# Optimization experiments

Measured on AMD Instinct MI355X. Metric: run time of the kernel, lower is better.

Reference implementation:

```python
import jax, jax.numpy as jnp
import numpy as np

DIM = 768
ALL_KEY_DIM = 768
NUM_HEADS = 12
HEAD_DIM = DIM // NUM_HEADS
SCALE = HEAD_DIM ** -0.5


def setup_inputs() -> dict:
    key = jax.random.key(0)
    ks = jax.random.split(key, 8)
    B, N = 8, 1024
    s = 0.02
    return {
        "x": jax.random.normal(ks[0], (B, N, DIM), dtype=jnp.float32),
        "Wq": jax.random.normal(ks[1], (ALL_KEY_DIM, DIM), dtype=jnp.float32) * s,
        "Wk": jax.random.normal(ks[2], (ALL_KEY_DIM, DIM), dtype=jnp.float32) * s,
        "Wv": jax.random.normal(ks[3], (DIM, DIM), dtype=jnp.float32) * s,
        "bv": jnp.zeros((DIM,), dtype=jnp.float32),
        "Wmix": jax.random.normal(ks[4], (NUM_HEADS, ALL_KEY_DIM), dtype=jnp.float32) * s,
        "Wcb": jax.random.normal(ks[5], (NUM_HEADS, DIM), dtype=jnp.float32) * s,
        "Wproj": jax.random.normal(ks[6], (DIM, DIM), dtype=jnp.float32) * s,
        "bproj": jnp.zeros((DIM,), dtype=jnp.float32),
    }


def reference(x, Wq, Wk, Wv, bv, Wmix, Wcb, Wproj, bproj):
    B, N, C = x.shape
    H, Dh = NUM_HEADS, C // NUM_HEADS
    q_shared = x @ Wq.T                      # [B,N,Dk]
    k = x @ Wk.T                             # [B,N,Dk]
    v = (x @ Wv.T + bv).reshape(B, N, H, Dh).transpose(0, 2, 1, 3)  # [B,H,N,Dh]
    # per-head mixed query: q[b,h,n,d] = q_shared[b,n,d] * Wmix[h,d]
    q = jnp.einsum('bnd,hd->bhnd', q_shared, Wmix)
    # shared-key scores + content bias broadcast over query positions
    scores = jnp.einsum('bhnd,bmd->bhnm', q, k)          # [B,H,N,N]
    content_bias = jnp.einsum('bmd,hd->bhm', x, Wcb)     # [B,H,N]
    attn = jax.nn.softmax((scores + content_bias[:, :, None, :]) * SCALE, axis=-1)
    out = jnp.einsum('bhnm,bhmd->bhnd', attn, v)         # [B,H,N,Dh]
    out = out.transpose(0, 2, 1, 3).reshape(B, N, C)
    return out @ Wproj.T + bproj
```

## Files before the change

kernel.cpp:

```cpp
#include <hip/hip_runtime.h>
#include <stdint.h>

typedef unsigned short u16;
typedef unsigned char u8;
typedef unsigned long long u64;
typedef __attribute__((ext_vector_type(8))) short bf16x8;
typedef __attribute__((ext_vector_type(4))) float f32x4;

#define KLOG2E 0.18033688011112043f
#define QSCL 184.66496523378732f
#define SINV 0.0001220703125f
#define EXP2F(x) __builtin_amdgcn_exp2f(x)
#define WAITV(n) asm volatile("s_waitcnt vmcnt(" #n ")" ::: "memory")

__device__ __forceinline__ u16 f2bf(float f) {
  union { float f; unsigned u; } v; v.f = f;
  unsigned r = v.u + 0x7fffu + ((v.u >> 16) & 1u);
  return (u16)(r >> 16);
}
__device__ __forceinline__ float bf2f(u16 u) {
  union { unsigned u; float f; } v; v.u = ((unsigned)u) << 16;
  return v.f;
}
__device__ __forceinline__ u8 f2fp8(float f) {
  return (u8)(__builtin_amdgcn_cvt_pk_fp8_f32(f, f, 0, false) & 0xFF);
}
__device__ __forceinline__ long pk64(uint2 v) {
  return (long)(((u64)v.y << 32) | (u64)v.x);
}

__device__ __forceinline__ void gload16(const void* g, void* l) {
  __builtin_amdgcn_global_load_lds(
      (const __attribute__((address_space(1))) unsigned int*)g,
      (__attribute__((address_space(3))) unsigned int*)l, 16, 0, 0);
}

__global__ void cvt_f32_bf16(const float4* __restrict__ s, uint2* __restrict__ d, int n4) {
  int i = blockIdx.x * blockDim.x + threadIdx.x;
  int stride = gridDim.x * blockDim.x;
  for (; i < n4; i += stride) {
    float4 v = s[i];
    uint2 o;
    o.x = (unsigned)f2bf(v.x) | ((unsigned)f2bf(v.y) << 16);
    o.y = (unsigned)f2bf(v.z) | ((unsigned)f2bf(v.w) << 16);
    d[i] = o;
  }
}

template <int MODE>
__global__ __launch_bounds__(256, 2) void gemm_bt(
    const u16* __restrict__ A, const u16* __restrict__ Bm,
    void* __restrict__ Cp, void* __restrict__ Cp2,
    const float* __restrict__ bias, int ldc) {
  __shared__ u16 Ab[128 * 32];
  __shared__ u16 Bb[128 * 32];
  const int tid = threadIdx.x;
  const int l = tid & 63, w = tid >> 6;
  const int g = l >> 4, l15 = l & 15;
  const int wr = w >> 1, wc = w & 1;
  const int rowbase = blockIdx.y * 128, colbase = blockIdx.x * 128;

  f32x4 acc[4][4] = {};
  const char* Abase = (const char*)A + (size_t)rowbase * 1536;
  const char* Bbase = (const char*)Bm + (size_t)colbase * 1536;

  for (int kk = 0; kk < 768; kk += 32) {
    __syncthreads();
#pragma unroll
    for (int p = 0; p < 2; ++p) {
      int o = p * 4096 + w * 1024 + l * 16;
      int row = o >> 6, cb = o & 63;
      gload16(Abase + (size_t)row * 1536 + kk * 2 + cb, &Ab[(p * 4096 + w * 1024) / 2]);
      gload16(Bbase + (size_t)row * 1536 + kk * 2 + cb, &Bb[(p * 4096 + w * 1024) / 2]);
    }
    __syncthreads();
    bf16x8 af[4], bfr[4];
#pragma unroll
    for (int i = 0; i < 4; ++i) {
      af[i] = *(const bf16x8*)&Ab[(wr * 64 + i * 16 + l15) * 32 + g * 8];
      bfr[i] = *(const bf16x8*)&Bb[(wc * 64 + i * 16 + l15) * 32 + g * 8];
    }
#pragma unroll
    for (int mi = 0; mi < 4; ++mi)
#pragma unroll
      for (int ni = 0; ni < 4; ++ni)
        acc[mi][ni] = __builtin_amdgcn_mfma_f32_16x16x32_bf16(af[mi], bfr[ni], acc[mi][ni], 0, 0, 0);
  }

#pragma unroll
  for (int mi = 0; mi < 4; ++mi)
#pragma unroll
    for (int ni = 0; ni < 4; ++ni)
#pragma unroll
      for (int r = 0; r < 4; ++r) {
        int row = rowbase + wr * 64 + mi * 16 + g * 4 + r;
        int col = colbase + wc * 64 + ni * 16 + l15;
        float v = acc[mi][ni][r];
        if (MODE == 0) {
          if (col < 768) {
            ((u16*)Cp)[(size_t)row * 768 + col] = f2bf(v);
          } else {
            int d = col - 768;
            int chunk = d >> 7, w4 = (d >> 5) & 3, gg = (d >> 3) & 3, rr = d & 7;
            int dp = chunk * 128 + gg * 32 + w4 * 8 + rr;
            ((u8*)Cp2)[(size_t)row * 768 + dp] = f2fp8(v * 8.0f);
          }
        } else if (MODE == 2) {
          ((float*)Cp)[(size_t)row * ldc + col] = v + bias[col];
        } else {
          int b = col >> 10, nn = col & 1023;
          if (row < 768) {
            ((u16*)Cp)[(size_t)b * 786432 + (size_t)row * 1024 + nn] = f2bf(v + bias[row]);
          } else if (row < 780) {
            ((float*)Cp2)[(size_t)b * 12288 + (size_t)(row - 768) * 1024 + nn] = v * KLOG2E;
          }
        }
      }
}

__global__ __launch_bounds__(512, 6) void attn8(
    const u16* __restrict__ Qb,
    const u8* __restrict__ Kf8,
    const u16* __restrict__ vT,
    const float* __restrict__ cb,
    const float* __restrict__ Wmix,
    u16* __restrict__ OH)
{
  __shared__ u8 Kb[3][8192];
  __shared__ u16 Vb[2][4096];
  __shared__ u16 Pb[8][1024];

  const int gid = blockIdx.x;
  const int b = gid & 7;
  const int within = gid >> 3;
  const int h = within % 12, qt = within / 12;
  const int tid = threadIdx.x;
  const int l = tid & 63, w = tid >> 6;
  const int g = l >> 4, l15 = l & 15;

  const u8* Ksrc = Kf8 + (size_t)b * 786432;
  const char* Vsrc = (const char*)vT + (size_t)(b * 12 + h) * 131072;
  const float* cbp = cb + (size_t)(b * 12 + h) * 1024;

  uint2 qreg[24];
  {
    const u16* qrow = Qb + ((size_t)b * 1024 + qt * 128 + w * 16 + l15) * 768;
    const float* wmh = Wmix + h * 768;
#pragma unroll
    for (int wd = 0; wd < 24; ++wd) {
      bf16x8 qv = *(const bf16x8*)(qrow + wd * 32 + g * 8);
      const float* wm = wmh + wd * 32 + g * 8;
      float4 w0 = *(const float4*)wm;
      float4 w1 = *(const float4*)(wm + 4);
      float q0 = bf2f((u16)qv[0]) * (w0.x * QSCL);
      float q1 = bf2f((u16)qv[1]) * (w0.y * QSCL);
      float q2 = bf2f((u16)qv[2]) * (w0.z * QSCL);
      float q3 = bf2f((u16)qv[3]) * (w0.w * QSCL);
      float q4 = bf2f((u16)qv[4]) * (w1.x * QSCL);
      float q5 = bf2f((u16)qv[5]) * (w1.y * QSCL);
      float q6 = bf2f((u16)qv[6]) * (w1.z * QSCL);
      float q7 = bf2f((u16)qv[7]) * (w1.w * QSCL);
      int a = __builtin_amdgcn_cvt_pk_fp8_f32(q0, q1, 0, false);
      a = __builtin_amdgcn_cvt_pk_fp8_f32(q2, q3, a, true);
      int b2 = __builtin_amdgcn_cvt_pk_fp8_f32(q4, q5, 0, false);
      b2 = __builtin_amdgcn_cvt_pk_fp8_f32(q6, q7, b2, true);
      qreg[wd].x = (unsigned)a;
      qreg[wd].y = (unsigned)b2;
    }
  }

  auto STK = [&](int kt, int ch, int buf) {
    int o = tid * 16;
    int row = o >> 7, t = (o >> 4) & 7;
    gload16(Ksrc + (size_t)(kt * 64 + row) * 768 + ch * 128 + ((t ^ (row & 7)) * 16),
            (char*)Kb[buf] + o);
  };
  auto STV = [&](int kt, int buf) {
    int o = tid * 16;
    int kwin = o >> 12, o2 = o & 4095, d = o2 >> 6, s = (o2 >> 4) & 3;
    gload16(Vsrc + (size_t)d * 2048 + (kt * 64 + kwin * 32 + ((s ^ (d & 3)) * 8)) * 2,
            (char*)Vb[buf] + o);
  };

  float m_run = -1e30f, lpart = 0.f;
  f32x4 oacc[4] = {};
  STK(0, 0, 0);
  STK(0, 1, 1);
  STV(0, 0);
  __syncthreads();

  for (int kt = 0; kt < 16; ++kt) {
    f32x4 sa[4] = {};
#pragma unroll
    for (int ch = 0; ch < 6; ++ch) {
      if (ch == 1 && kt < 15) STV(kt + 1, (kt + 1) & 1);
      if (ch <= 3) STK(kt, ch + 2, (ch + 2) % 3);
      else if (kt < 15) STK(kt + 1, ch - 4, (ch + 2) % 3);
      __builtin_amdgcn_s_setprio(1);
#pragma unroll
      for (int j = 0; j < 2; ++j) {
        long qf0 = pk64(qreg[ch * 4 + 2 * j]);
        long qf1 = pk64(qreg[ch * 4 + 2 * j + 1]);
        int slot = (2 * g + j) ^ (l15 & 7);
#pragma unroll
        for (int s = 0; s < 4; ++s) {
          uint4 kk = *(const uint4*)&Kb[ch % 3][(16 * s + l15) * 128 + slot * 16];
          long klo = (long)(((u64)kk.y << 32) | kk.x);
          long khi = (long)(((u64)kk.w << 32) | kk.z);
          sa[s] = __builtin_amdgcn_mfma_f32_16x16x32_fp8_fp8(klo, qf0, sa[s], 0, 0, 0);
          sa[s] = __builtin_amdgcn_mfma_f32_16x16x32_fp8_fp8(khi, qf1, sa[s], 0, 0, 0);
        }
      }
      __builtin_amdgcn_s_setprio(0);
      if (ch == 1) {
        if (kt < 15) WAITV(2); else WAITV(1);
      } else if (ch >= 4) {
        if (kt < 15) WAITV(1); else WAITV(0);
      } else {
        WAITV(1);
      }
      __builtin_amdgcn_s_barrier();
    }

    float fv[16];
    float pmax = -1e30f;
#pragma unroll
    for (int s = 0; s < 4; ++s) {
      float4 cbv = *(const float4*)(cbp + kt * 64 + s * 16 + g * 4);
      fv[s * 4 + 0] = fmaf(sa[s][0], SINV, cbv.x);
      fv[s * 4 + 1] = fmaf(sa[s][1], SINV, cbv.y);
      fv[s * 4 + 2] = fmaf(sa[s][2], SINV, cbv.z);
      fv[s * 4 + 3] = fmaf(sa[s][3], SINV, cbv.w);
#pragma unroll
      for (int r = 0; r < 4; ++r) pmax = fmaxf(pmax, fv[s * 4 + r]);
    }
    pmax = fmaxf(pmax, __shfl_xor(pmax, 16));
    pmax = fmaxf(pmax, __shfl_xor(pmax, 32));
    if (__ballot(pmax > m_run)) {
      float mnew = fmaxf(m_run, pmax);
      float alpha = EXP2F(m_run - mnew);
      lpart *= alpha;
#pragma unroll
      for (int vf = 0; vf < 4; ++vf) oacc[vf] *= alpha;
      m_run = mnew;
    }
    float rs = 0.f;
#pragma unroll
    for (int r = 0; r < 16; ++r) {
      fv[r] = EXP2F(fv[r] - m_run);
      rs += fv[r];
    }
    rs += __shfl_xor(rs, 16);
    rs += __shfl_xor(rs, 32);
    lpart += rs;

#pragma unroll
    for (int s = 0; s < 4; ++s) {
      unsigned w01, w23;
      asm("v_cvt_pk_bf16_f32 %0, %1, %2" : "=v"(w01) : "v"(fv[s * 4]), "v"(fv[s * 4 + 1]));
      asm("v_cvt_pk_bf16_f32 %0, %1, %2" : "=v"(w23) : "v"(fv[s * 4 + 2]), "v"(fv[s * 4 + 3]));
      int ts = (2 * s + (g >> 1)) ^ (l15 & 7);
      uint2 uu; uu.x = w01; uu.y = w23;
      *(uint2*)((char*)Pb[w] + l15 * 128 + ts * 16 + (g & 1) * 8) = uu;
    }

#pragma unroll
    for (int kwin = 0; kwin < 2; ++kwin) {
      int tr = (4 * kwin + g) ^ (l15 & 7);
      bf16x8 pf = *(const bf16x8*)((const char*)Pb[w] + l15 * 128 + tr * 16);
#pragma unroll
      for (int vf = 0; vf < 4; ++vf) {
        int d = vf * 16 + l15;
        bf16x8 vfrag = *(const bf16x8*)((const char*)Vb[kt & 1] + kwin * 4096 + d * 64 +
                                        ((g ^ (d & 3)) * 16));
        oacc[vf] = __builtin_amdgcn_mfma_f32_16x16x32_bf16(vfrag, pf, oacc[vf], 0, 0, 0);
      }
    }
  }

  float rdiv = 1.f / lpart;
  size_t nrow = ((size_t)b * 1024 + qt * 128 + w * 16 + l15) * 768;
#pragma unroll
  for (int vf = 0; vf < 4; ++vf) {
    u64 pk = (u64)f2bf(oacc[vf][0] * rdiv) |
             ((u64)f2bf(oacc[vf][1] * rdiv) << 16) |
             ((u64)f2bf(oacc[vf][2] * rdiv) << 32) |
             ((u64)f2bf(oacc[vf][3] * rdiv) << 48);
    *(u64*)&OH[nrow + h * 64 + vf * 16 + 4 * g] = pk;
  }
}

static inline int cvtblocks(int n4) {
  int nb = (n4 + 255) / 256;
  return nb > 2048 ? 2048 : nb;
}

extern "C" void kernel_launch(void* const* d_in, const int* in_sizes, int n_in,
                              void* d_out, int out_size, void* d_ws, size_t ws_size,
                              hipStream_t stream) {
  (void)in_sizes; (void)n_in; (void)out_size; (void)ws_size;
  const float* x = (const float*)d_in[0];
  const float* Wq = (const float*)d_in[1];
  const float* Wk = (const float*)d_in[2];
  const float* Wv = (const float*)d_in[3];
  const float* bv = (const float*)d_in[4];
  const float* Wmix = (const float*)d_in[5];
  const float* Wcb = (const float*)d_in[6];
  const float* Wproj = (const float*)d_in[7];
  const float* bproj = (const float*)d_in[8];
  float* out = (float*)d_out;

  char* ws = (char*)d_ws;
  u16* xbf = (u16*)(ws);
  u16* Wqk = (u16*)(ws + 12582912);
  u16* Wvcb = (u16*)(ws + 14942208);
  u16* Wpj = (u16*)(ws + 16318464);
  u16* Qb = (u16*)(ws + 17498112);
  u8* Kf8 = (u8*)(ws + 30081024);
  u16* vT = (u16*)(ws + 36372480);
  float* cbb = (float*)(ws + 48955392);
  u16* OH = (u16*)(ws + 49348608);

  cvt_f32_bf16<<<cvtblocks(1572864), 256, 0, stream>>>((const float4*)x, (uint2*)xbf, 1572864);
  cvt_f32_bf16<<<cvtblocks(147456), 256, 0, stream>>>((const float4*)Wq, (uint2*)Wqk, 147456);
  cvt_f32_bf16<<<cvtblocks(147456), 256, 0, stream>>>((const float4*)Wk, (uint2*)(Wqk + 589824), 147456);
  cvt_f32_bf16<<<cvtblocks(147456), 256, 0, stream>>>((const float4*)Wv, (uint2*)Wvcb, 147456);
  cvt_f32_bf16<<<cvtblocks(2304), 256, 0, stream>>>((const float4*)Wcb, (uint2*)(Wvcb + 589824), 2304);
  cvt_f32_bf16<<<cvtblocks(147456), 256, 0, stream>>>((const float4*)Wproj, (uint2*)Wpj, 147456);

  gemm_bt<0><<<dim3(12, 64), 256, 0, stream>>>(xbf, Wqk, Qb, Kf8, nullptr, 0);
  gemm_bt<1><<<dim3(64, 7), 256, 0, stream>>>(Wvcb, xbf, vT, cbb, bv, 0);
  attn8<<<dim3(768), 512, 0, stream>>>(Qb, Kf8, vT, cbb, Wmix, OH);
  gemm_bt<2><<<dim3(6, 64), 256, 0, stream>>>(OH, Wpj, out, nullptr, bproj, 768);
}
```

Measured before the change: 246.2 us.

## Rewrite attention with 32x32 scaled fp8 and bf16 MFMAs in registers

```diff
diff --git a/kernel.cpp b/kernel.cpp
--- a/kernel.cpp
+++ b/kernel.cpp
@@ -6,6 +6,8 @@
 typedef unsigned long long u64;
 typedef __attribute__((ext_vector_type(8))) short bf16x8;
 typedef __attribute__((ext_vector_type(4))) float f32x4;
+typedef __attribute__((ext_vector_type(16))) float f32x16;
+typedef __attribute__((ext_vector_type(8))) int i32x8;
 
 #define KLOG2E 0.18033688011112043f
 #define QSCL 184.66496523378732f
@@ -24,9 +26,6 @@
 }
 __device__ __forceinline__ u8 f2fp8(float f) {
   return (u8)(__builtin_amdgcn_cvt_pk_fp8_f32(f, f, 0, false) & 0xFF);
-}
-__device__ __forceinline__ long pk64(uint2 v) {
-  return (long)(((u64)v.y << 32) | (u64)v.x);
 }
 
 __device__ __forceinline__ void gload16(const void* g, void* l) {
@@ -100,10 +99,7 @@
           if (col < 768) {
             ((u16*)Cp)[(size_t)row * 768 + col] = f2bf(v);
           } else {
-            int d = col - 768;
-            int chunk = d >> 7, w4 = (d >> 5) & 3, gg = (d >> 3) & 3, rr = d & 7;
-            int dp = chunk * 128 + gg * 32 + w4 * 8 + rr;
-            ((u8*)Cp2)[(size_t)row * 768 + dp] = f2fp8(v * 8.0f);
+            ((u8*)Cp2)[(size_t)row * 768 + (col - 768)] = f2fp8(v * 8.0f);
           }
         } else if (MODE == 2) {
           ((float*)Cp)[(size_t)row * ldc + col] = v + bias[col];
@@ -118,7 +114,7 @@
       }
 }
 
-__global__ __launch_bounds__(512, 6) void attn8(
+__global__ __launch_bounds__(256, 2) void attn9(
     const u16* __restrict__ Qb,
     const u8* __restrict__ Kf8,
     const u16* __restrict__ vT,
@@ -128,166 +124,196 @@
 {
   __shared__ u8 Kb[3][8192];
   __shared__ u16 Vb[2][4096];
-  __shared__ u16 Pb[8][1024];
 
   const int gid = blockIdx.x;
   const int b = gid & 7;
   const int within = gid >> 3;
   const int h = within % 12, qt = within / 12;
   const int tid = threadIdx.x;
-  const int l = tid & 63, w = tid >> 6;
-  const int g = l >> 4, l15 = l & 15;
+  const int lane = tid & 63, w = tid >> 6;
+  const int c = lane & 31, hi = lane >> 5;
 
   const u8* Ksrc = Kf8 + (size_t)b * 786432;
   const char* Vsrc = (const char*)vT + (size_t)(b * 12 + h) * 131072;
   const float* cbp = cb + (size_t)(b * 12 + h) * 1024;
 
-  uint2 qreg[24];
-  {
-    const u16* qrow = Qb + ((size_t)b * 1024 + qt * 128 + w * 16 + l15) * 768;
-    const float* wmh = Wmix + h * 768;
-#pragma unroll
-    for (int wd = 0; wd < 24; ++wd) {
-      bf16x8 qv = *(const bf16x8*)(qrow + wd * 32 + g * 8);
-      const float* wm = wmh + wd * 32 + g * 8;
-      float4 w0 = *(const float4*)wm;
-      float4 w1 = *(const float4*)(wm + 4);
-      float q0 = bf2f((u16)qv[0]) * (w0.x * QSCL);
-      float q1 = bf2f((u16)qv[1]) * (w0.y * QSCL);
-      float q2 = bf2f((u16)qv[2]) * (w0.z * QSCL);
-      float q3 = bf2f((u16)qv[3]) * (w0.w * QSCL);
-      float q4 = bf2f((u16)qv[4]) * (w1.x * QSCL);
-      float q5 = bf2f((u16)qv[5]) * (w1.y * QSCL);
-      float q6 = bf2f((u16)qv[6]) * (w1.z * QSCL);
-      float q7 = bf2f((u16)qv[7]) * (w1.w * QSCL);
-      int a = __builtin_amdgcn_cvt_pk_fp8_f32(q0, q1, 0, false);
-      a = __builtin_amdgcn_cvt_pk_fp8_f32(q2, q3, a, true);
-      int b2 = __builtin_amdgcn_cvt_pk_fp8_f32(q4, q5, 0, false);
-      b2 = __builtin_amdgcn_cvt_pk_fp8_f32(q6, q7, b2, true);
-      qreg[wd].x = (unsigned)a;
-      qreg[wd].y = (unsigned)b2;
-    }
-  }
-
-  auto STK = [&](int kt, int ch, int buf) {
-    int o = tid * 16;
-    int row = o >> 7, t = (o >> 4) & 7;
-    gload16(Ksrc + (size_t)(kt * 64 + row) * 768 + ch * 128 + ((t ^ (row & 7)) * 16),
-            (char*)Kb[buf] + o);
+  auto STK = [&](int kt2, int ch2, int buf) {
+#pragma unroll
+    for (int p4 = 0; p4 < 2; ++p4) {
+      int o = p4 * 4096 + tid * 16;
+      int row = o >> 7, t = (o >> 4) & 7;
+      gload16(Ksrc + (size_t)(kt2 * 64 + row) * 768 + ch2 * 128 + ((t ^ (row & 7)) * 16),
+              (char*)Kb[buf] + o);
+    }
   };
-  auto STV = [&](int kt, int buf) {
-    int o = tid * 16;
-    int kwin = o >> 12, o2 = o & 4095, d = o2 >> 6, s = (o2 >> 4) & 3;
-    gload16(Vsrc + (size_t)d * 2048 + (kt * 64 + kwin * 32 + ((s ^ (d & 3)) * 8)) * 2,
-            (char*)Vb[buf] + o);
+  auto STV = [&](int kt2, int buf) {
+#pragma unroll
+    for (int p4 = 0; p4 < 2; ++p4) {
+      int o = p4 * 4096 + tid * 16;
+      int row = o >> 7, t = (o >> 4) & 7;
+      gload16(Vsrc + (size_t)row * 2048 + kt2 * 128 + ((t ^ (row & 7)) * 16),
+              (char*)Vb[buf] + o);
+    }
   };
 
-  float m_run = -1e30f, lpart = 0.f;
-  f32x4 oacc[4] = {};
   STK(0, 0, 0);
   STK(0, 1, 1);
   STV(0, 0);
-  __syncthreads();
+
+  i32x8 qreg[12];
+  {
+    const u16* qrow = Qb + ((size_t)b * 1024 + qt * 128 + w * 32 + c) * 768;
+    const float* wmh = Wmix + h * 768;
+#pragma unroll
+    for (int D = 0; D < 12; ++D) {
+      i32x8 qq;
+#pragma unroll
+      for (int j = 0; j < 4; ++j) {
+        int off = D * 64 + hi * 32 + j * 8;
+        bf16x8 qv = *(const bf16x8*)(qrow + off);
+        float4 w0 = *(const float4*)(wmh + off);
+        float4 w1 = *(const float4*)(wmh + off + 4);
+        float q0 = bf2f((u16)qv[0]) * (w0.x * QSCL);
+        float q1 = bf2f((u16)qv[1]) * (w0.y * QSCL);
+        float q2 = bf2f((u16)qv[2]) * (w0.z * QSCL);
+        float q3 = bf2f((u16)qv[3]) * (w0.w * QSCL);
+        float q4 = bf2f((u16)qv[4]) * (w1.x * QSCL);
+        float q5 = bf2f((u16)qv[5]) * (w1.y * QSCL);
+        float q6 = bf2f((u16)qv[6]) * (w1.z * QSCL);
+        float q7 = bf2f((u16)qv[7]) * (w1.w * QSCL);
+        int a = __builtin_amdgcn_cvt_pk_fp8_f32(q0, q1, 0, false);
+        a = __builtin_amdgcn_cvt_pk_fp8_f32(q2, q3, a, true);
+        int b2 = __builtin_amdgcn_cvt_pk_fp8_f32(q4, q5, 0, false);
+        b2 = __builtin_amdgcn_cvt_pk_fp8_f32(q6, q7, b2, true);
+        qq[2 * j] = a;
+        qq[2 * j + 1] = b2;
+      }
+      qreg[D] = qq;
+    }
+  }
+
+  WAITV(4);
+  __builtin_amdgcn_s_barrier();
+
+  float m_run = -1e30f, lpart = 0.f;
+  f32x16 oacc[2] = {};
 
   for (int kt = 0; kt < 16; ++kt) {
-    f32x4 sa[4] = {};
+    float4 cv[8];
+#pragma unroll
+    for (int kg = 0; kg < 2; ++kg)
+#pragma unroll
+      for (int j = 0; j < 4; ++j)
+        cv[kg * 4 + j] = *(const float4*)(cbp + kt * 64 + kg * 32 + 8 * j + 4 * hi);
+
+    f32x16 sa[2] = {};
 #pragma unroll
     for (int ch = 0; ch < 6; ++ch) {
-      if (ch == 1 && kt < 15) STV(kt + 1, (kt + 1) & 1);
       if (ch <= 3) STK(kt, ch + 2, (ch + 2) % 3);
       else if (kt < 15) STK(kt + 1, ch - 4, (ch + 2) % 3);
+      if (ch == 3 && kt < 15) STV(kt + 1, (kt + 1) & 1);
+
       __builtin_amdgcn_s_setprio(1);
-#pragma unroll
-      for (int j = 0; j < 2; ++j) {
-        long qf0 = pk64(qreg[ch * 4 + 2 * j]);
-        long qf1 = pk64(qreg[ch * 4 + 2 * j + 1]);
-        int slot = (2 * g + j) ^ (l15 & 7);
-#pragma unroll
-        for (int s = 0; s < 4; ++s) {
-          uint4 kk = *(const uint4*)&Kb[ch % 3][(16 * s + l15) * 128 + slot * 16];
-          long klo = (long)(((u64)kk.y << 32) | kk.x);
-          long khi = (long)(((u64)kk.w << 32) | kk.z);
-          sa[s] = __builtin_amdgcn_mfma_f32_16x16x32_fp8_fp8(klo, qf0, sa[s], 0, 0, 0);
-          sa[s] = __builtin_amdgcn_mfma_f32_16x16x32_fp8_fp8(khi, qf1, sa[s], 0, 0, 0);
+      const u8* kbuf = Kb[ch % 3];
+#pragma unroll
+      for (int dblk = 0; dblk < 2; ++dblk) {
+        const int D = ch * 2 + dblk;
+#pragma unroll
+        for (int kg = 0; kg < 2; ++kg) {
+          int r = kg * 32 + c;
+          int s0 = dblk * 4 + hi * 2;
+          const u8* kb = kbuf + r * 128;
+          uint4 klo = *(const uint4*)(kb + ((s0 ^ (r & 7)) * 16));
+          uint4 khi4 = *(const uint4*)(kb + (((s0 + 1) ^ (r & 7)) * 16));
+          i32x8 af;
+          af[0] = (int)klo.x; af[1] = (int)klo.y; af[2] = (int)klo.z; af[3] = (int)klo.w;
+          af[4] = (int)khi4.x; af[5] = (int)khi4.y; af[6] = (int)khi4.z; af[7] = (int)khi4.w;
+          sa[kg] = __builtin_amdgcn_mfma_scale_f32_32x32x64_f8f6f4(
+              af, qreg[D], sa[kg], 0, 0, 0, 127, 0, 127);
         }
       }
       __builtin_amdgcn_s_setprio(0);
-      if (ch == 1) {
-        if (kt < 15) WAITV(2); else WAITV(1);
-      } else if (ch >= 4) {
-        if (kt < 15) WAITV(1); else WAITV(0);
-      } else {
-        WAITV(1);
-      }
+
+      if (ch == 0) { if (kt == 0) { WAITV(4); } else { WAITV(2); } }
+      else if (ch == 1 || ch == 2) { WAITV(2); }
+      else if (ch == 3) { if (kt < 15) { WAITV(4); } else { WAITV(2); } }
+      else if (ch == 4) { if (kt < 15) { WAITV(4); } else { WAITV(0); } }
+      else { if (kt < 15) { WAITV(2); } else { WAITV(0); } }
       __builtin_amdgcn_s_barrier();
     }
 
-    float fv[16];
+    float fv[32];
     float pmax = -1e30f;
 #pragma unroll
-    for (int s = 0; s < 4; ++s) {
-      float4 cbv = *(const float4*)(cbp + kt * 64 + s * 16 + g * 4);
-      fv[s * 4 + 0] = fmaf(sa[s][0], SINV, cbv.x);
-      fv[s * 4 + 1] = fmaf(sa[s][1], SINV, cbv.y);
-      fv[s * 4 + 2] = fmaf(sa[s][2], SINV, cbv.z);
-      fv[s * 4 + 3] = fmaf(sa[s][3], SINV, cbv.w);
-#pragma unroll
-      for (int r = 0; r < 4; ++r) pmax = fmaxf(pmax, fv[s * 4 + r]);
-    }
-    pmax = fmaxf(pmax, __shfl_xor(pmax, 16));
+    for (int kg = 0; kg < 2; ++kg)
+#pragma unroll
+      for (int u = 0; u < 16; ++u) {
+        float cbv = ((const float*)&cv[kg * 4 + (u >> 2)])[u & 3];
+        float t = fmaf(sa[kg][u], SINV, cbv);
+        fv[kg * 16 + u] = t;
+        pmax = fmaxf(pmax, t);
+      }
     pmax = fmaxf(pmax, __shfl_xor(pmax, 32));
     if (__ballot(pmax > m_run)) {
       float mnew = fmaxf(m_run, pmax);
       float alpha = EXP2F(m_run - mnew);
       lpart *= alpha;
-#pragma unroll
-      for (int vf = 0; vf < 4; ++vf) oacc[vf] *= alpha;
+      oacc[0] *= alpha;
+      oacc[1] *= alpha;
       m_run = mnew;
     }
     float rs = 0.f;
 #pragma unroll
-    for (int r = 0; r < 16; ++r) {
-      fv[r] = EXP2F(fv[r] - m_run);
-      rs += fv[r];
-    }
-    rs += __shfl_xor(rs, 16);
+    for (int u2 = 0; u2 < 32; ++u2) {
+      fv[u2] = EXP2F(fv[u2] - m_run);
+      rs += fv[u2];
+    }
     rs += __shfl_xor(rs, 32);
     lpart += rs;
 
 #pragma unroll
-    for (int s = 0; s < 4; ++s) {
-      unsigned w01, w23;
-      asm("v_cvt_pk_bf16_f32 %0, %1, %2" : "=v"(w01) : "v"(fv[s * 4]), "v"(fv[s * 4 + 1]));
-      asm("v_cvt_pk_bf16_f32 %0, %1, %2" : "=v"(w23) : "v"(fv[s * 4 + 2]), "v"(fv[s * 4 + 3]));
-      int ts = (2 * s + (g >> 1)) ^ (l15 & 7);
-      uint2 uu; uu.x = w01; uu.y = w23;
-      *(uint2*)((char*)Pb[w] + l15 * 128 + ts * 16 + (g & 1) * 8) = uu;
-    }
-
-#pragma unroll
-    for (int kwin = 0; kwin < 2; ++kwin) {
-      int tr = (4 * kwin + g) ^ (l15 & 7);
-      bf16x8 pf = *(const bf16x8*)((const char*)Pb[w] + l15 * 128 + tr * 16);
-#pragma unroll
-      for (int vf = 0; vf < 4; ++vf) {
-        int d = vf * 16 + l15;
-        bf16x8 vfrag = *(const bf16x8*)((const char*)Vb[kt & 1] + kwin * 4096 + d * 64 +
-                                        ((g ^ (d & 3)) * 16));
-        oacc[vf] = __builtin_amdgcn_mfma_f32_16x16x32_bf16(vfrag, pf, oacc[vf], 0, 0, 0);
-      }
+    for (int kg = 0; kg < 2; ++kg) {
+      const float* pv = &fv[kg * 16];
+      bf16x8 pf[2];
+#pragma unroll
+      for (int win = 0; win < 2; ++win) {
+        unsigned xw, yw, zw, tw;
+        asm("v_cvt_pk_bf16_f32 %0, %1, %2" : "=v"(xw) : "v"(pv[win * 8 + 0]), "v"(pv[win * 8 + 1]));
+        asm("v_cvt_pk_bf16_f32 %0, %1, %2" : "=v"(yw) : "v"(pv[win * 8 + 2]), "v"(pv[win * 8 + 3]));
+        asm("v_cvt_pk_bf16_f32 %0, %1, %2" : "=v"(zw) : "v"(pv[win * 8 + 4]), "v"(pv[win * 8 + 5]));
+        asm("v_cvt_pk_bf16_f32 %0, %1, %2" : "=v"(tw) : "v"(pv[win * 8 + 6]), "v"(pv[win * 8 + 7]));
+        asm volatile("v_permlane32_swap_b32 %0, %1" : "+v"(xw), "+v"(zw));
+        asm volatile("v_permlane32_swap_b32 %0, %1" : "+v"(yw), "+v"(tw));
+        union { unsigned u[4]; bf16x8 v; } bu;
+        bu.u[0] = xw; bu.u[1] = yw; bu.u[2] = zw; bu.u[3] = tw;
+        pf[win] = bu.v;
+      }
+#pragma unroll
+      for (int win = 0; win < 2; ++win)
+#pragma unroll
+        for (int dg = 0; dg < 2; ++dg) {
+          int rd = dg * 32 + c;
+          int sv = kg * 4 + win * 2 + hi;
+          bf16x8 vf = *(const bf16x8*)((const char*)Vb[kt & 1] + rd * 128 +
+                                       ((sv ^ (rd & 7)) * 16));
+          oacc[dg] = __builtin_amdgcn_mfma_f32_32x32x16_bf16(vf, pf[win], oacc[dg], 0, 0, 0);
+        }
     }
   }
 
   float rdiv = 1.f / lpart;
-  size_t nrow = ((size_t)b * 1024 + qt * 128 + w * 16 + l15) * 768;
-#pragma unroll
-  for (int vf = 0; vf < 4; ++vf) {
-    u64 pk = (u64)f2bf(oacc[vf][0] * rdiv) |
-             ((u64)f2bf(oacc[vf][1] * rdiv) << 16) |
-             ((u64)f2bf(oacc[vf][2] * rdiv) << 32) |
-             ((u64)f2bf(oacc[vf][3] * rdiv) << 48);
-    *(u64*)&OH[nrow + h * 64 + vf * 16 + 4 * g] = pk;
-  }
+  int n = qt * 128 + w * 32 + c;
+  size_t nrow = ((size_t)b * 1024 + n) * 768 + h * 64;
+#pragma unroll
+  for (int dg = 0; dg < 2; ++dg)
+#pragma unroll
+    for (int j = 0; j < 4; ++j) {
+      u64 pk = (u64)f2bf(oacc[dg][4 * j + 0] * rdiv) |
+               ((u64)f2bf(oacc[dg][4 * j + 1] * rdiv) << 16) |
+               ((u64)f2bf(oacc[dg][4 * j + 2] * rdiv) << 32) |
+               ((u64)f2bf(oacc[dg][4 * j + 3] * rdiv) << 48);
+      *(u64*)&OH[nrow + dg * 32 + 8 * j + 4 * hi] = pk;
+    }
 }
 
 static inline int cvtblocks(int n4) {
@@ -330,6 +356,6 @@
 
   gemm_bt<0><<<dim3(12, 64), 256, 0, stream>>>(xbf, Wqk, Qb, Kf8, nullptr, 0);
   gemm_bt<1><<<dim3(64, 7), 256, 0, stream>>>(Wvcb, xbf, vT, cbb, bv, 0);
-  attn8<<<dim3(768), 512, 0, stream>>>(Qb, Kf8, vT, cbb, Wmix, OH);
+  attn9<<<dim3(768), 256, 0, stream>>>(Qb, Kf8, vT, cbb, Wmix, OH);
   gemm_bt<2><<<dim3(6, 64), 256, 0, stream>>>(OH, Wpj, out, nullptr, bproj, 768);
 }
```

Measured after the change: 618.8 us. +151.3%, slower.

## Double-buffer K tiles, stage content bias in LDS, issue loads before Q prep

Applied to the files above, without the earlier changes.

```diff
diff --git a/kernel.cpp b/kernel.cpp
--- a/kernel.cpp
+++ b/kernel.cpp
@@ -33,6 +33,11 @@
   __builtin_amdgcn_global_load_lds(
       (const __attribute__((address_space(1))) unsigned int*)g,
       (__attribute__((address_space(3))) unsigned int*)l, 16, 0, 0);
+}
+__device__ __forceinline__ void gload4(const void* g, void* l) {
+  __builtin_amdgcn_global_load_lds(
+      (const __attribute__((address_space(1))) unsigned int*)g,
+      (__attribute__((address_space(3))) unsigned int*)l, 4, 0, 0);
 }
 
 __global__ void cvt_f32_bf16(const float4* __restrict__ s, uint2* __restrict__ d, int n4) {
@@ -118,7 +123,7 @@
       }
 }
 
-__global__ __launch_bounds__(512, 6) void attn8(
+__global__ __launch_bounds__(512, 6) void attn13(
     const u16* __restrict__ Qb,
     const u8* __restrict__ Kf8,
     const u16* __restrict__ vT,
@@ -126,9 +131,10 @@
     const float* __restrict__ Wmix,
     u16* __restrict__ OH)
 {
-  __shared__ u8 Kb[3][8192];
+  __shared__ u8 Kb[2][8192];
   __shared__ u16 Vb[2][4096];
   __shared__ u16 Pb[8][1024];
+  __shared__ float cbL[1024];
 
   const int gid = blockIdx.x;
   const int b = gid & 7;
@@ -141,6 +147,25 @@
   const u8* Ksrc = Kf8 + (size_t)b * 786432;
   const char* Vsrc = (const char*)vT + (size_t)(b * 12 + h) * 131072;
   const float* cbp = cb + (size_t)(b * 12 + h) * 1024;
+
+  auto STK = [&](int kt, int ch, int buf) {
+    int o = tid * 16;
+    int row = o >> 7, t = (o >> 4) & 7;
+    gload16(Ksrc + (size_t)(kt * 64 + row) * 768 + ch * 128 + ((t ^ (row & 7)) * 16),
+            (char*)Kb[buf] + o);
+  };
+  auto STV = [&](int kt, int buf) {
+    int o = tid * 16;
+    int kwin = o >> 12, o2 = o & 4095, d = o2 >> 6, s = (o2 >> 4) & 3;
+    gload16(Vsrc + (size_t)d * 2048 + (kt * 64 + kwin * 32 + ((s ^ (d & 3)) * 8)) * 2,
+            (char*)Vb[buf] + o);
+  };
+
+  gload4(cbp + tid, (char*)cbL + ((tid >> 6) << 8));
+  gload4(cbp + 512 + tid, (char*)(cbL + 512) + ((tid >> 6) << 8));
+  STK(0, 0, 0);
+  STK(0, 1, 1);
+  STV(0, 0);
 
   uint2 qreg[24];
   {
@@ -169,33 +194,22 @@
     }
   }
 
-  auto STK = [&](int kt, int ch, int buf) {
-    int o = tid * 16;
-    int row = o >> 7, t = (o >> 4) & 7;
-    gload16(Ksrc + (size_t)(kt * 64 + row) * 768 + ch * 128 + ((t ^ (row & 7)) * 16),
-            (char*)Kb[buf] + o);
-  };
-  auto STV = [&](int kt, int buf) {
-    int o = tid * 16;
-    int kwin = o >> 12, o2 = o & 4095, d = o2 >> 6, s = (o2 >> 4) & 3;
-    gload16(Vsrc + (size_t)d * 2048 + (kt * 64 + kwin * 32 + ((s ^ (d & 3)) * 8)) * 2,
-            (char*)Vb[buf] + o);
-  };
+  WAITV(0);
+  __builtin_amdgcn_s_barrier();
 
   float m_run = -1e30f, lpart = 0.f;
   f32x4 oacc[4] = {};
-  STK(0, 0, 0);
-  STK(0, 1, 1);
-  STV(0, 0);
-  __syncthreads();
-
+
+#pragma unroll 1
   for (int kt = 0; kt < 16; ++kt) {
     f32x4 sa[4] = {};
 #pragma unroll
     for (int ch = 0; ch < 6; ++ch) {
+      if (ch == 0) { if (kt > 0) STK(kt, 1, 1); }
+      else if (ch < 5) STK(kt, ch + 1, (ch + 1) & 1);
+      else if (kt < 15) STK(kt + 1, 0, 0);
       if (ch == 1 && kt < 15) STV(kt + 1, (kt + 1) & 1);
-      if (ch <= 3) STK(kt, ch + 2, (ch + 2) % 3);
-      else if (kt < 15) STK(kt + 1, ch - 4, (ch + 2) % 3);
+
       __builtin_amdgcn_s_setprio(1);
 #pragma unroll
       for (int j = 0; j < 2; ++j) {
@@ -204,7 +218,7 @@
         int slot = (2 * g + j) ^ (l15 & 7);
 #pragma unroll
         for (int s = 0; s < 4; ++s) {
-          uint4 kk = *(const uint4*)&Kb[ch % 3][(16 * s + l15) * 128 + slot * 16];
+          uint4 kk = *(const uint4*)&Kb[ch & 1][(16 * s + l15) * 128 + slot * 16];
           long klo = (long)(((u64)kk.y << 32) | kk.x);
           long khi = (long)(((u64)kk.w << 32) | kk.z);
           sa[s] = __builtin_amdgcn_mfma_f32_16x16x32_fp8_fp8(klo, qf0, sa[s], 0, 0, 0);
@@ -212,13 +226,11 @@
         }
       }
       __builtin_amdgcn_s_setprio(0);
-      if (ch == 1) {
-        if (kt < 15) WAITV(2); else WAITV(1);
-      } else if (ch >= 4) {
-        if (kt < 15) WAITV(1); else WAITV(0);
-      } else {
-        WAITV(1);
-      }
+
+      if (ch == 0) { if (kt == 0) { WAITV(0); } else { WAITV(1); } }
+      else if (ch == 1) { if (kt < 15) { WAITV(2); } else { WAITV(1); } }
+      else if (ch <= 4) { if (kt < 15) { WAITV(2); } else { WAITV(1); } }
+      else { if (kt < 15) { WAITV(2); } else { WAITV(0); } }
       __builtin_amdgcn_s_barrier();
     }
 
@@ -226,7 +238,7 @@
     float pmax = -1e30f;
 #pragma unroll
     for (int s = 0; s < 4; ++s) {
-      float4 cbv = *(const float4*)(cbp + kt * 64 + s * 16 + g * 4);
+      float4 cbv = *(const float4*)&cbL[kt * 64 + s * 16 + g * 4];
       fv[s * 4 + 0] = fmaf(sa[s][0], SINV, cbv.x);
       fv[s * 4 + 1] = fmaf(sa[s][1], SINV, cbv.y);
       fv[s * 4 + 2] = fmaf(sa[s][2], SINV, cbv.z);
@@ -330,6 +342,6 @@
 
   gemm_bt<0><<<dim3(12, 64), 256, 0, stream>>>(xbf, Wqk, Qb, Kf8, nullptr, 0);
   gemm_bt<1><<<dim3(64, 7), 256, 0, stream>>>(Wvcb, xbf, vT, cbb, bv, 0);
-  attn8<<<dim3(768), 512, 0, stream>>>(Qb, Kf8, vT, cbb, Wmix, OH);
+  attn13<<<dim3(768), 512, 0, stream>>>(Qb, Kf8, vT, cbb, Wmix, OH);
   gemm_bt<2><<<dim3(6, 64), 256, 0, stream>>>(OH, Wpj, out, nullptr, bproj, 768);
 }
```

After: 303.8 us. +23.4%, slower.
